# Kernel tuning notes

Hardware: AMD Instinct MI355X
Metric: run time of the kernel (lower is better)

## Reference

```python
import jax, jax.numpy as jnp
import numpy as np

N = 8192          # points
M = 3             # point dimension
K_ORDER = 4       # tensor order k
C = 64            # input_in_channel
KNN = 16          # n_neighbors
NEG_SLOPE = 0.2
EPS = 1e-6


def vn_leaky_relu(v, U, neg_slope=NEG_SLOPE, eps=EPS):
    """Vector-neuron LeakyReLU. v: (n, T, C), U: (C, C) learned direction map."""
    d = jnp.einsum('ntc,cd->ntd', v, U)
    dot = jnp.sum(v * d, axis=1, keepdims=True)        # (n,1,C)
    dn2 = jnp.sum(d * d, axis=1, keepdims=True)        # (n,1,C)
    proj = (dot / (dn2 + eps)) * d
    return neg_slope * v + (1.0 - neg_slope) * jnp.where(dot >= 0, v, v - proj)


def contract_pairs(x, w, k):
    """Learned combination of all pairwise traces.
    x: (n, m,...,m (k axes), C); w: (k*(k-1)//2, C). Returns order k-2 tensor."""
    pairs = [(a, b) for a in range(1, k + 1) for b in range(a + 1, k + 1)]
    acc = None
    for i, (a, b) in enumerate(pairs):
        t = jnp.trace(x, axis1=a, axis2=b)             # (n, m^(k-2)..., C)
        acc = t * w[i] if acc is None else acc + t * w[i]
    return acc


def setup_inputs() -> dict:
    key = jax.random.key(0)
    ks = jax.random.split(key, 8)
    s1 = 1.0 / np.sqrt(C)
    s2 = 1.0 / np.sqrt(2 * C)
    return {
        'x': jax.random.normal(ks[0], (N, M), dtype=jnp.float32),
        'kron_W': jax.random.normal(ks[1], (K_ORDER, C, C), dtype=jnp.float32) * s1,
        'kron_U': jax.random.normal(ks[2], (K_ORDER, C, C), dtype=jnp.float32) * s1,
        'contr_w4': jax.random.normal(ks[3], (6, 2 * C), dtype=jnp.float32) * s2,
        'contr_W': jax.random.normal(ks[4], (2 * C, 2 * C), dtype=jnp.float32) * s2,
        'contr_U': jax.random.normal(ks[5], (2 * C, 2 * C), dtype=jnp.float32) * s2,
        'contr_w2': jax.random.normal(ks[6], (1, 2 * C), dtype=jnp.float32) * s2,
    }


def reference(x, kron_W, kron_U, contr_w4, contr_W, contr_U, contr_w2):
    n, m = x.shape
    c = kron_W.shape[-1]
    # --- brute-force kNN on x (replaces sklearn fit/kneighbors; self included,
    # static because dynamic_knn=False) ---
    sq = jnp.sum(x * x, axis=1)
    d2 = sq[:, None] + sq[None, :] - 2.0 * (x @ x.T)   # (n,n)
    _, idx = jax.lax.top_k(-d2, KNN)                   # (n,KNN) neighbor indices
    xg = x[idx]                                        # (n,KNN,m) gathered coords
    # --- Kronecker stage: v_{t+1}[i] = mean_{j in N(i)} x_j (x) v_t[j] ---
    v = jnp.ones((n, 1, c), dtype=x.dtype)
    for t in range(kron_W.shape[0]):
        vg = v[idx]                                    # (n,KNN,m^t,c)
        v = jnp.einsum('nka,nkbc->nabc', xg, vg) / KNN # (n,m,m^t,c)
        v = v.reshape(n, -1, c)                        # (n,m^(t+1),c)
        v = v @ kron_W[t]                              # CustomLinear (no bias)
        v = vn_leaky_relu(v, kron_U[t])
    # --- mean pooling + concat (pool_type=mean) ---
    g = jnp.mean(v, axis=0, keepdims=True)
    v = jnp.concatenate([v, jnp.broadcast_to(g, v.shape)], axis=2)  # (n,m^k,2c)
    c2 = 2 * c
    k = kron_W.shape[0]
    h = v.reshape((n,) + (m,) * k + (c2,))             # (n,3,3,3,3,2c)
    # --- contraction stage: k=4 -> 2 -> 0 ---
    h = contract_pairs(h, contr_w4, k)                 # (n,m,m,2c)
    h = h.reshape(n, m * m, c2) @ contr_W              # CustomLinear
    h = vn_leaky_relu(h, contr_U)
    h = h.reshape(n, m, m, c2)
    out = contract_pairs(h, contr_w2, 2)               # (n,2c)
    return out
```

## Files before the change

kernel.cpp:

```cpp
#include <hip/hip_runtime.h>
#include <math.h>

#define NPTS 8192
#define KNB  16
#define C1   64
#define C2   128
#define NEG  0.2f
#define VEPS 1e-6f
#define NCH  32
#define CHSZ (NPTS/NCH)

__device__ __forceinline__ unsigned long long expand10(unsigned v) {
    unsigned long long r = v & 0x3FFu;
    r = (r | (r << 16)) & 0x030000FFULL;
    r = (r | (r <<  8)) & 0x0300F00FULL;
    r = (r | (r <<  4)) & 0x030C30C3ULL;
    r = (r | (r <<  2)) & 0x09249249ULL;
    return r;
}

__global__ __launch_bounds__(256) void keys_kernel(const float* __restrict__ x,
                                                   unsigned long long* __restrict__ keys)
{
    const int i = blockIdx.x * 256 + threadIdx.x;
    auto cell = [](float v) -> unsigned {
        float t = (v + 6.f) * (1024.f / 12.f);
        int c = (int)t;
        c = c < 0 ? 0 : (c > 1023 ? 1023 : c);
        return (unsigned)c;
    };
    const unsigned long long m = expand10(cell(x[3*i+0]))
                               | (expand10(cell(x[3*i+1])) << 1)
                               | (expand10(cell(x[3*i+2])) << 2);
    keys[i] = (m << 13) | (unsigned long long)i;
}

__global__ __launch_bounds__(256) void rank_zero(int* __restrict__ rk)
{
    rk[blockIdx.x * 256 + threadIdx.x] = 0;
}

__global__ __launch_bounds__(256) void rank_part(const unsigned long long* __restrict__ keys,
                                                 int* __restrict__ rk)
{
    __shared__ unsigned long long sk[1024];
    const int slice = blockIdx.x & 7;
    const int qg    = blockIdx.x >> 3;
    for (int j = threadIdx.x; j < 1024; j += 256) sk[j] = keys[slice*1024 + j];
    __syncthreads();
    const int i = qg*256 + threadIdx.x;
    const unsigned long long mine = keys[i];
    int r = 0;
    for (int j = 0; j < 1024; j += 4)
        r += (int)(sk[j] < mine) + (int)(sk[j+1] < mine)
           + (int)(sk[j+2] < mine) + (int)(sk[j+3] < mine);
    atomicAdd(&rk[i], r);
}

__global__ __launch_bounds__(256) void rank_scatter(const int* __restrict__ rk,
                                                    const float* __restrict__ x,
                                                    float* __restrict__ xp,
                                                    int* __restrict__ perm)
{
    const int i = blockIdx.x * 256 + threadIdx.x;
    const int r = rk[i];
    perm[r] = i;
    xp[3*r+0] = x[3*i+0]; xp[3*r+1] = x[3*i+1]; xp[3*r+2] = x[3*i+2];
}

__global__ __launch_bounds__(256) void knn_part(const float* __restrict__ x,
                                                unsigned long long* __restrict__ parts)
{
    __shared__ __align__(16) float4 cpt[CHSZ];
    __shared__ unsigned long long sbuf[256 * 9];

    const int tid   = threadIdx.x;
    const int chunk = blockIdx.x & (NCH - 1);
    const int qg    = blockIdx.x >> 5;
    const int j0    = chunk * CHSZ;

    cpt[tid] = make_float4(x[3*(j0+tid)+0], x[3*(j0+tid)+1], x[3*(j0+tid)+2], 0.f);
    const int q = qg * 256 + tid;
    const float qx = x[3*q+0], qy = x[3*q+1], qz = x[3*q+2];

    float thrF;
    {
        int lo = q - 7; lo = lo < 0 ? 0 : (lo > NPTS-16 ? NPTS-16 : lo);
        float mx = 0.f;
#pragma unroll
        for (int s = 0; s < 16; ++s) {
            const float dx = qx - x[3*(lo+s)+0];
            const float dy = qy - x[3*(lo+s)+1];
            const float dz = qz - x[3*(lo+s)+2];
            mx = fmaxf(mx, fmaf(dx, dx, fmaf(dy, dy, dz*dz)));
        }
        thrF = mx * 1.0002f;
    }
    __syncthreads();

    unsigned long long bd[16];
#pragma unroll
    for (int r = 0; r < 16; ++r) bd[r] = ~0ull;
    int cnt = 0;
    unsigned long long* mybuf = sbuf + tid * 9;

    auto flush = [&]() {
#pragma unroll
        for (int s = 0; s < 8; ++s) {
            if (s < cnt) {
                const unsigned long long k = mybuf[s];
                if (k < bd[15]) {
#pragma unroll
                    for (int p2 = 15; p2 > 0; --p2) {
                        const bool sh = k < bd[p2-1];
                        const bool pl = k < bd[p2];
                        bd[p2] = sh ? bd[p2-1] : (pl ? k : bd[p2]);
                    }
                    if (k < bd[0]) bd[0] = k;
                }
            }
        }
        cnt = 0;
        if (bd[15] != ~0ull) {
            const double dub = __longlong_as_double((long long)(bd[15] | 8191ull));
            thrF = fminf(thrF, (float)dub * 1.0001f);
        }
    };

    for (int jj = 0; jj < CHSZ; jj += 4) {
        const float4 p0 = cpt[jj+0];
        const float4 p1 = cpt[jj+1];
        const float4 p2 = cpt[jj+2];
        const float4 p3 = cpt[jj+3];
#pragma unroll
        for (int u = 0; u < 4; ++u) {
            const float4 p = (u==0) ? p0 : (u==1) ? p1 : (u==2) ? p2 : p3;
            const float dx = qx - p.x, dy = qy - p.y, dz = qz - p.z;
            const float d2f = fmaf(dx, dx, fmaf(dy, dy, dz*dz));
            if (d2f <= thrF) {
                const double ddx = (double)dx, ddy = (double)dy, ddz = (double)dz;
                const double d2 = ddx*ddx + ddy*ddy + ddz*ddz;
                const unsigned long long key =
                    (((unsigned long long)__double_as_longlong(d2)) & ~8191ull)
                    | (unsigned long long)(j0 + jj + u);
                if (key < bd[15]) { mybuf[cnt] = key; ++cnt; }
            }
        }
        if (__any(cnt >= 5)) flush();
    }
    flush();

#pragma unroll
    for (int r = 0; r < 16; ++r)
        parts[((size_t)chunk * KNB + r) * NPTS + q] = bd[r];
}

__global__ __launch_bounds__(256) void knn_merge(const unsigned long long* __restrict__ parts,
                                                 int* __restrict__ idx_out)
{
    __shared__ unsigned char heads[256][NCH];
    const int tid = threadIdx.x;
    const int q = blockIdx.x * 256 + tid;
    unsigned char* h = heads[tid];
#pragma unroll
    for (int c = 0; c < NCH; ++c) h[c] = 0;
    for (int r = 0; r < KNB; ++r) {
        unsigned long long best = ~0ull; int bc = 0;
#pragma unroll
        for (int c = 0; c < NCH; ++c) {
            const unsigned long long k = parts[((size_t)c * KNB + h[c]) * NPTS + q];
            if (k < best) { best = k; bc = c; }
        }
        h[bc]++;
        idx_out[q*KNB + r] = (int)(best & 8191ull);
    }
}

__global__ __launch_bounds__(256) void prep_kernel(const float* __restrict__ kW,
                                                   const float* __restrict__ kU,
                                                   float* __restrict__ scol,
                                                   float* __restrict__ bcat)
{
    __shared__ float sW[64*64];
    __shared__ float sS[64];
    const int t = blockIdx.x;
    const int tid = threadIdx.x;
    if (t == 0) {
        for (int e = tid; e < 64*64; e += 256) sW[e] = kW[e];
        __syncthreads();
        if (tid < 64) {
            float s = 0.f;
            for (int j = 0; j < 64; ++j) s += sW[j*64 + tid];
            sS[tid] = s;
        }
        __syncthreads();
        if (tid < 64) {
            float s2 = 0.f;
            for (int j = 0; j < 64; ++j) s2 = fmaf(sS[j], kU[j*64 + tid], s2);
            scol[tid]      = sS[tid];
            scol[64 + tid] = s2;
        }
    } else {
        const float* W = kW + t*4096;
        const float* U = kU + t*4096;
        for (int e = tid; e < 64*64; e += 256) sW[e] = W[e];
        __syncthreads();
        float* B = bcat + (size_t)(t-1)*64*128;
        for (int o = tid; o < 64*64; o += 256) {
            const int j = o >> 6, c = o & 63;
            float s = 0.f;
            for (int l = 0; l < 64; ++l) s = fmaf(sW[j*64 + l], U[l*64 + c], s);
            B[j*128 + c]      = sW[j*64 + c];
            B[j*128 + 64 + c] = s;
        }
    }
}

__global__ __launch_bounds__(256) void step1_kernel(const float* __restrict__ xp,
                                                    const int* __restrict__ idxs,
                                                    const float* __restrict__ scol,
                                                    float* __restrict__ R1)
{
    const int pt = blockIdx.x * 256 + threadIdx.x;
    float mx0 = 0.f, mx1 = 0.f, mx2 = 0.f;
#pragma unroll
    for (int k = 0; k < KNB; ++k) {
        const int id = idxs[pt*KNB + k];
        mx0 += xp[3*id+0]; mx1 += xp[3*id+1]; mx2 += xp[3*id+2];
    }
    const float inv = 1.0f / KNB;
    mx0 *= inv; mx1 *= inv; mx2 *= inv;
    const float S2 = mx0*mx0 + mx1*mx1 + mx2*mx2;
    float* op = R1 + (size_t)pt * 192;
    for (int c = 0; c < 64; ++c) {
        const float sc = scol[c], su = scol[64 + c];
        const float dt = S2 * sc * su;
        const float dn = S2 * su * su;
        const float m  = (dt < 0.f) ? 0.8f * dt / (dn + VEPS) : 0.f;
        const float rc = fmaf(-m, su, sc);
        op[c]       = mx0 * rc;
        op[64 + c]  = mx1 * rc;
        op[128 + c] = mx2 * rc;
    }
}

#define FMA4(ar, b0, b1, b2, b3, acc) \
    acc.x = fmaf(ar.x,b0.x, fmaf(ar.y,b1.x, fmaf(ar.z,b2.x, fmaf(ar.w,b3.x, acc.x)))); \
    acc.y = fmaf(ar.x,b0.y, fmaf(ar.y,b1.y, fmaf(ar.z,b2.y, fmaf(ar.w,b3.y, acc.y)))); \
    acc.z = fmaf(ar.x,b0.z, fmaf(ar.y,b1.z, fmaf(ar.z,b2.z, fmaf(ar.w,b3.z, acc.z)))); \
    acc.w = fmaf(ar.x,b0.w, fmaf(ar.y,b1.w, fmaf(ar.z,b2.w, fmaf(ar.w,b3.w, acc.w))));

__global__ __launch_bounds__(256) void zgemm_kernel(const float* __restrict__ R,
                                                    const float* __restrict__ Bcat,
                                                    float* __restrict__ YwZ)
{
    constexpr int SA = 68;
    __shared__ __align__(16) float sA[64*SA];
    __shared__ __align__(16) float sB[64*128];
    const int tid = threadIdx.x;
    const size_t row0 = (size_t)blockIdx.x * 64;

    for (int e4 = tid; e4 < 1024; e4 += 256) {
        const int r = e4 >> 4, c4 = (e4 & 15) * 4;
        *reinterpret_cast<float4*>(sA + r*SA + c4) =
            *reinterpret_cast<const float4*>(R + (row0 + r)*64 + c4);
    }
    for (int e4 = tid; e4 < 2048; e4 += 256) {
        const int j = e4 >> 5, c4 = (e4 & 31) * 4;
        *reinterpret_cast<float4*>(sB + j*128 + c4) =
            *reinterpret_cast<const float4*>(Bcat + j*128 + c4);
    }
    __syncthreads();

    const int rg = tid >> 5;
    const int d  = (tid & 31) * 4;
    float4 acc0={0,0,0,0},acc1=acc0,acc2=acc0,acc3=acc0,acc4=acc0,acc5=acc0,acc6=acc0,acc7=acc0;
    for (int c = 0; c < 64; c += 4) {
        const float4 b0 = *reinterpret_cast<const float4*>(sB + (c+0)*128 + d);
        const float4 b1 = *reinterpret_cast<const float4*>(sB + (c+1)*128 + d);
        const float4 b2 = *reinterpret_cast<const float4*>(sB + (c+2)*128 + d);
        const float4 b3 = *reinterpret_cast<const float4*>(sB + (c+3)*128 + d);
        float4 a;
        a = *reinterpret_cast<const float4*>(sA + (rg*8+0)*SA + c); FMA4(a,b0,b1,b2,b3,acc0);
        a = *reinterpret_cast<const float4*>(sA + (rg*8+1)*SA + c); FMA4(a,b0,b1,b2,b3,acc1);
        a = *reinterpret_cast<const float4*>(sA + (rg*8+2)*SA + c); FMA4(a,b0,b1,b2,b3,acc2);
        a = *reinterpret_cast<const float4*>(sA + (rg*8+3)*SA + c); FMA4(a,b0,b1,b2,b3,acc3);
        a = *reinterpret_cast<const float4*>(sA + (rg*8+4)*SA + c); FMA4(a,b0,b1,b2,b3,acc4);
        a = *reinterpret_cast<const float4*>(sA + (rg*8+5)*SA + c); FMA4(a,b0,b1,b2,b3,acc5);
        a = *reinterpret_cast<const float4*>(sA + (rg*8+6)*SA + c); FMA4(a,b0,b1,b2,b3,acc6);
        a = *reinterpret_cast<const float4*>(sA + (rg*8+7)*SA + c); FMA4(a,b0,b1,b2,b3,acc7);
    }
    float* op = YwZ + (row0 + rg*8)*128 + d;
    *reinterpret_cast<float4*>(op + 0*128) = acc0;
    *reinterpret_cast<float4*>(op + 1*128) = acc1;
    *reinterpret_cast<float4*>(op + 2*128) = acc2;
    *reinterpret_cast<float4*>(op + 3*128) = acc3;
    *reinterpret_cast<float4*>(op + 4*128) = acc4;
    *reinterpret_cast<float4*>(op + 5*128) = acc5;
    *reinterpret_cast<float4*>(op + 6*128) = acc6;
    *reinterpret_cast<float4*>(op + 7*128) = acc7;
}

template<int PINP, int TT>
__global__ __launch_bounds__(256) void gather_kernel(
    const float* __restrict__ xp, const int* __restrict__ idxs,
    const float* __restrict__ yz,
    float* __restrict__ Rout,
    int ppb)
{
    constexpr int PCW = PINP * 128;
    constexpr int NSL = PCW / 4;
    constexpr int TC  = TT * 64;

    __shared__ __align__(16) float buf[TT * 128];
    __shared__ int   sIds[KNB];
    __shared__ float sXg[KNB*3];
    __shared__ float pdt[4][64], pdn[4][64], msc[64];

    const int tid   = threadIdx.x;
    const int slots = gridDim.x >> 3;
    const int xcd   = blockIdx.x & 7;
    const int slot  = blockIdx.x >> 3;
    const int base  = xcd * slots * ppb;

    for (int pi = 0; pi < ppb; ++pi) {
        const int pt = base + pi * slots + slot;
        if (tid < KNB) {
            const int id = idxs[pt*KNB + tid];
            sIds[tid] = id;
            sXg[tid*3+0] = xp[3*id+0];
            sXg[tid*3+1] = xp[3*id+1];
            sXg[tid*3+2] = xp[3*id+2];
        }
        __syncthreads();

        float xr[KNB*3];
#pragma unroll
        for (int e = 0; e < KNB*3; ++e) xr[e] = sXg[e];

        for (int sl = tid; sl < NSL; sl += 256) {
            const int b  = sl >> 5;
            const int cc = (sl & 31) * 4;
            float4 s0 = {0,0,0,0}, s1 = s0, s2 = s0;
#pragma unroll
            for (int k = 0; k < KNB; ++k) {
                const float4 val = *reinterpret_cast<const float4*>(
                    yz + (size_t)sIds[k]*PCW + b*128 + cc);
                const float xa = xr[k*3+0], xb = xr[k*3+1], xc = xr[k*3+2];
                s0.x=fmaf(xa,val.x,s0.x); s0.y=fmaf(xa,val.y,s0.y);
                s0.z=fmaf(xa,val.z,s0.z); s0.w=fmaf(xa,val.w,s0.w);
                s1.x=fmaf(xb,val.x,s1.x); s1.y=fmaf(xb,val.y,s1.y);
                s1.z=fmaf(xb,val.z,s1.z); s1.w=fmaf(xb,val.w,s1.w);
                s2.x=fmaf(xc,val.x,s2.x); s2.y=fmaf(xc,val.y,s2.y);
                s2.z=fmaf(xc,val.z,s2.z); s2.w=fmaf(xc,val.w,s2.w);
            }
            const float inv = 1.0f / KNB;
            s0.x*=inv; s0.y*=inv; s0.z*=inv; s0.w*=inv;
            s1.x*=inv; s1.y*=inv; s1.z*=inv; s1.w*=inv;
            s2.x*=inv; s2.y*=inv; s2.z*=inv; s2.w*=inv;
            *reinterpret_cast<float4*>(buf + (0*PINP + b)*128 + cc) = s0;
            *reinterpret_cast<float4*>(buf + (1*PINP + b)*128 + cc) = s1;
            *reinterpret_cast<float4*>(buf + (2*PINP + b)*128 + cc) = s2;
        }
        __syncthreads();
        {
            const int c = tid & 63, g = tid >> 6;
            float dt = 0.f, dn = 0.f;
            for (int t = g; t < TT; t += 4) {
                const float vv = buf[t*128 + c], dd = buf[t*128 + 64 + c];
                dt = fmaf(vv, dd, dt); dn = fmaf(dd, dd, dn);
            }
            pdt[g][c] = dt; pdn[g][c] = dn;
        }
        __syncthreads();
        if (tid < 64) {
            const float dt = pdt[0][tid]+pdt[1][tid]+pdt[2][tid]+pdt[3][tid];
            const float dn = pdn[0][tid]+pdn[1][tid]+pdn[2][tid]+pdn[3][tid];
            msc[tid] = (dt < 0.f) ? 0.8f * dt / (dn + VEPS) : 0.f;
        }
        __syncthreads();
        {
            float* op = Rout + (size_t)pt * TC;
            for (int e = tid; e < TC; e += 256) {
                const int t = e >> 6, c = e & 63;
                op[e] = fmaf(-msc[c], buf[t*128 + 64 + c], buf[t*128 + c]);
            }
        }
        __syncthreads();
    }
}

__global__ __launch_bounds__(256) void gather4_kernel(
    const float* __restrict__ xp, const int* __restrict__ idxs,
    const float* __restrict__ yz,
    const float* __restrict__ w4,
    float* __restrict__ hv, float* __restrict__ gpart,
    int ppb)
{
    constexpr int TT = 81;
    constexpr int CH = 32;
    constexpr int NG = (TT*CH + 255) / 256;

    __shared__ __align__(16) float buf[TT * 64];
    __shared__ int   sIds[KNB];
    __shared__ float sXg[KNB*3];
    __shared__ float pdt[8][CH], pdn[8][CH], msc[CH];

    const int tid   = threadIdx.x;
    const int xcd   = blockIdx.x & 7;
    const int r2    = blockIdx.x >> 3;
    const int half  = r2 & 1;
    const int slot  = r2 >> 1;
    const int slots = gridDim.x >> 4;
    const int base0 = xcd * slots * ppb;
    const int c0    = half * CH;
    const int eff   = xcd * slots + slot;

    float gacc[NG];
#pragma unroll
    for (int i = 0; i < NG; ++i) gacc[i] = 0.f;

    for (int pi = 0; pi < ppb; ++pi) {
        const int pt = base0 + pi * slots + slot;
        if (tid < KNB) {
            const int id = idxs[pt*KNB + tid];
            sIds[tid] = id;
            sXg[tid*3+0] = xp[3*id+0];
            sXg[tid*3+1] = xp[3*id+1];
            sXg[tid*3+2] = xp[3*id+2];
        }
        __syncthreads();

        float xr[KNB*3];
#pragma unroll
        for (int e = 0; e < KNB*3; ++e) xr[e] = sXg[e];

        for (int sl = tid; sl < 27*16; sl += 256) {
            const int b  = sl >> 4;
            const int qq = sl & 15;
            const int src = b*128 + ((qq < 8) ? (c0 + qq*4) : (64 + c0 + (qq-8)*4));
            const int dst = (qq < 8) ? qq*4 : (32 + (qq-8)*4);
            float4 s0 = {0,0,0,0}, s1 = s0, s2 = s0;
#pragma unroll
            for (int k = 0; k < KNB; ++k) {
                const float4 val = *reinterpret_cast<const float4*>(
                    yz + (size_t)sIds[k]*3456 + src);
                const float xa = xr[k*3+0], xb = xr[k*3+1], xc = xr[k*3+2];
                s0.x=fmaf(xa,val.x,s0.x); s0.y=fmaf(xa,val.y,s0.y);
                s0.z=fmaf(xa,val.z,s0.z); s0.w=fmaf(xa,val.w,s0.w);
                s1.x=fmaf(xb,val.x,s1.x); s1.y=fmaf(xb,val.y,s1.y);
                s1.z=fmaf(xb,val.z,s1.z); s1.w=fmaf(xb,val.w,s1.w);
                s2.x=fmaf(xc,val.x,s2.x); s2.y=fmaf(xc,val.y,s2.y);
                s2.z=fmaf(xc,val.z,s2.z); s2.w=fmaf(xc,val.w,s2.w);
            }
            const float inv = 1.0f / KNB;
            s0.x*=inv; s0.y*=inv; s0.z*=inv; s0.w*=inv;
            s1.x*=inv; s1.y*=inv; s1.z*=inv; s1.w*=inv;
            s2.x*=inv; s2.y*=inv; s2.z*=inv; s2.w*=inv;
            *reinterpret_cast<float4*>(buf + (0*27 + b)*64 + dst) = s0;
            *reinterpret_cast<float4*>(buf + (1*27 + b)*64 + dst) = s1;
            *reinterpret_cast<float4*>(buf + (2*27 + b)*64 + dst) = s2;
        }
        __syncthreads();
        {
            const int cc = tid & 31, g = tid >> 5;
            float dt = 0.f, dn = 0.f;
            for (int t = g; t < TT; t += 8) {
                const float vv = buf[t*64 + cc], dd = buf[t*64 + 32 + cc];
                dt = fmaf(vv, dd, dt); dn = fmaf(dd, dd, dn);
            }
            pdt[g][cc] = dt; pdn[g][cc] = dn;
        }
        __syncthreads();
        if (tid < CH) {
            float dt = 0.f, dn = 0.f;
#pragma unroll
            for (int g = 0; g < 8; ++g) { dt += pdt[g][tid]; dn += pdn[g][tid]; }
            msc[tid] = (dt < 0.f) ? 0.8f * dt / (dn + VEPS) : 0.f;
        }
        __syncthreads();
#pragma unroll
        for (int i = 0; i < NG; ++i) {
            const int e = i*256 + tid;
            if (e < TT*CH) {
                const int t = e >> 5, cc = e & 31;
                const float v = fmaf(-msc[cc], buf[t*64 + 32 + cc], buf[t*64 + cc]);
                buf[t*64 + cc] = v;
                gacc[i] += v;
            }
        }
        __syncthreads();
        for (int e = tid; e < 9*CH; e += 256) {
            const int pq = e >> 5, cc = e & 31;
            const int p = pq / 3, qq = pq - 3*p;
            const int c = c0 + cc;
            float tr0=0,tr1=0,tr2=0,tr3=0,tr4=0,tr5=0;
#pragma unroll
            for (int r = 0; r < 3; ++r) {
                tr0 += buf[(r*36 + p*3 + qq )*64 + cc];
                tr1 += buf[(r*30 + p*9 + qq )*64 + cc];
                tr2 += buf[(r*28 + p*9 + qq*3)*64 + cc];
                tr3 += buf[(p*27 + r*12 + qq )*64 + cc];
                tr4 += buf[(p*27 + r*10 + qq*3)*64 + cc];
                tr5 += buf[(p*27 + qq*9 + r*4 )*64 + cc];
            }
            hv[(size_t)pt*576 + pq*64 + c] =
                  w4[0*C2 + c]*tr0 + w4[1*C2 + c]*tr1 + w4[2*C2 + c]*tr2
                + w4[3*C2 + c]*tr3 + w4[4*C2 + c]*tr4 + w4[5*C2 + c]*tr5;
        }
        __syncthreads();
    }
    float* gp = gpart + (size_t)eff * 5184;
#pragma unroll
    for (int i = 0; i < NG; ++i) {
        const int e = i*256 + tid;
        if (e < TT*CH) {
            const int t = e >> 5, cc = e & 31;
            gp[t*64 + c0 + cc] = gacc[i];
        }
    }
}

__global__ __launch_bounds__(256) void reduce_g_kernel(const float* __restrict__ gpart,
                                                       float* __restrict__ g)
{
    __shared__ float red[256];
    const int el = threadIdx.x & 15, pg = threadIdx.x >> 4;
    const int e = blockIdx.x * 16 + el;
    float s = 0.f;
    for (int p = pg; p < 1024; p += 16) s += gpart[(size_t)p * (81*C1) + e];
    red[threadIdx.x] = s;
    __syncthreads();
    for (int st = 8; st > 0; st >>= 1) {
        if (pg < st) red[el + 16*pg] += red[el + 16*(pg+st)];
        __syncthreads();
    }
    if (pg == 0) g[e] = red[el] * (1.0f/NPTS);
}

__global__ __launch_bounds__(256) void hgw_kernel(const float* __restrict__ g,
                                                  const float* __restrict__ w4,
                                                  const float* __restrict__ cW,
                                                  float* __restrict__ hgW)
{
    __shared__ float gs[81*C1];
    __shared__ float hg[9*C1];
    const int tid = threadIdx.x;
    for (int e = tid; e < 81*C1; e += 256) gs[e] = g[e];
    __syncthreads();
    for (int e = tid; e < 9*C1; e += 256) {
        const int pq = e >> 6, c = e & 63;
        const int p = pq / 3, qq = pq - 3*p;
        float tr0=0,tr1=0,tr2=0,tr3=0,tr4=0,tr5=0;
#pragma unroll
        for (int r = 0; r < 3; ++r) {
            tr0 += gs[(r*36 + p*3 + qq ) * C1 + c];
            tr1 += gs[(r*30 + p*9 + qq ) * C1 + c];
            tr2 += gs[(r*28 + p*9 + qq*3) * C1 + c];
            tr3 += gs[(p*27 + r*12 + qq ) * C1 + c];
            tr4 += gs[(p*27 + r*10 + qq*3) * C1 + c];
            tr5 += gs[(p*27 + qq*9 + r*4 ) * C1 + c];
        }
        hg[e] = w4[0*C2 + 64 + c]*tr0 + w4[1*C2 + 64 + c]*tr1 + w4[2*C2 + 64 + c]*tr2
              + w4[3*C2 + 64 + c]*tr3 + w4[4*C2 + 64 + c]*tr4 + w4[5*C2 + 64 + c]*tr5;
    }
    __syncthreads();
    for (int o = tid; o < 9*C2; o += 256) {
        const int t = o >> 7, c = o & 127;
        float s = 0.f;
        for (int j = 0; j < C1; ++j) s = fmaf(hg[t*C1 + j], cW[(C1+j)*C2 + c], s);
        hgW[o] = s;
    }
}

__global__ __launch_bounds__(256) void contract_kernel(const float* __restrict__ hv,
                                                       const float* __restrict__ hgW,
                                                       const float* __restrict__ cW,
                                                       const float* __restrict__ cU,
                                                       const float* __restrict__ w2,
                                                       const int* __restrict__ perm,
                                                       float* __restrict__ out,
                                                       int ppb)
{
    constexpr int S0 = C1 + 4;
    constexpr int SH = C2 + 4;
    __shared__ __align__(16) float h0[36*S0];
    __shared__ __align__(16) float h1[36*SH];
    __shared__ __align__(16) float h2[36*SH];
    __shared__ __align__(16) float hgs[9*C2];
    __shared__ int sPerm[4];

    const int tid = threadIdx.x;
    for (int e = tid; e < 9*C2; e += 256) hgs[e] = hgW[e];
    __syncthreads();

    const int iters = ppb >> 2;
    for (int it = 0; it < iters; ++it) {
        const int base = blockIdx.x * ppb + it * 4;
        if (tid < 4) sPerm[tid] = perm[base + tid];
        for (int e = tid; e < 4*9*C1; e += 256) {
            const int pt = e / 576, rem = e - pt*576;
            const int t = rem >> 6, c = rem & 63;
            h0[(pt*9 + t)*S0 + c] = hv[(size_t)(base+pt)*576 + rem];
        }
        __syncthreads();
        for (int u = tid; u < 9*32; u += 256) {
            const int tg = u >> 5;
            const int d  = (u & 31) * 4;
            const int r0 = tg*4;
            float4 acc0 = *reinterpret_cast<const float4*>(hgs + ((r0+0)%9)*C2 + d);
            float4 acc1 = *reinterpret_cast<const float4*>(hgs + ((r0+1)%9)*C2 + d);
            float4 acc2 = *reinterpret_cast<const float4*>(hgs + ((r0+2)%9)*C2 + d);
            float4 acc3 = *reinterpret_cast<const float4*>(hgs + ((r0+3)%9)*C2 + d);
            for (int c = 0; c < C1; c += 4) {
                const float4 a0 = *reinterpret_cast<const float4*>(h0 + (r0+0)*S0 + c);
                const float4 a1 = *reinterpret_cast<const float4*>(h0 + (r0+1)*S0 + c);
                const float4 a2 = *reinterpret_cast<const float4*>(h0 + (r0+2)*S0 + c);
                const float4 a3 = *reinterpret_cast<const float4*>(h0 + (r0+3)*S0 + c);
                const float4 b0 = *reinterpret_cast<const float4*>(cW + (c+0)*C2 + d);
                const float4 b1 = *reinterpret_cast<const float4*>(cW + (c+1)*C2 + d);
                const float4 b2 = *reinterpret_cast<const float4*>(cW + (c+2)*C2 + d);
                const float4 b3 = *reinterpret_cast<const float4*>(cW + (c+3)*C2 + d);
                FMA4(a0, b0, b1, b2, b3, acc0);
                FMA4(a1, b0, b1, b2, b3, acc1);
                FMA4(a2, b0, b1, b2, b3, acc2);
                FMA4(a3, b0, b1, b2, b3, acc3);
            }
            *reinterpret_cast<float4*>(h1 + (r0+0)*SH + d) = acc0;
            *reinterpret_cast<float4*>(h1 + (r0+1)*SH + d) = acc1;
            *reinterpret_cast<float4*>(h1 + (r0+2)*SH + d) = acc2;
            *reinterpret_cast<float4*>(h1 + (r0+3)*SH + d) = acc3;
        }
        __syncthreads();
        for (int u = tid; u < 9*32; u += 256) {
            const int tg = u >> 5;
            const int d  = (u & 31) * 4;
            const int r0 = tg*4;
            float4 acc0 = {0,0,0,0}, acc1 = acc0, acc2 = acc0, acc3 = acc0;
            for (int c = 0; c < C2; c += 4) {
                const float4 a0 = *reinterpret_cast<const float4*>(h1 + (r0+0)*SH + c);
                const float4 a1 = *reinterpret_cast<const float4*>(h1 + (r0+1)*SH + c);
                const float4 a2 = *reinterpret_cast<const float4*>(h1 + (r0+2)*SH + c);
                const float4 a3 = *reinterpret_cast<const float4*>(h1 + (r0+3)*SH + c);
                const float4 b0 = *reinterpret_cast<const float4*>(cU + (c+0)*C2 + d);
                const float4 b1 = *reinterpret_cast<const float4*>(cU + (c+1)*C2 + d);
                const float4 b2 = *reinterpret_cast<const float4*>(cU + (c+2)*C2 + d);
                const float4 b3 = *reinterpret_cast<const float4*>(cU + (c+3)*C2 + d);
                FMA4(a0, b0, b1, b2, b3, acc0);
                FMA4(a1, b0, b1, b2, b3, acc1);
                FMA4(a2, b0, b1, b2, b3, acc2);
                FMA4(a3, b0, b1, b2, b3, acc3);
            }
            *reinterpret_cast<float4*>(h2 + (r0+0)*SH + d) = acc0;
            *reinterpret_cast<float4*>(h2 + (r0+1)*SH + d) = acc1;
            *reinterpret_cast<float4*>(h2 + (r0+2)*SH + d) = acc2;
            *reinterpret_cast<float4*>(h2 + (r0+3)*SH + d) = acc3;
        }
        __syncthreads();
#pragma unroll
        for (int p2 = 0; p2 < 2; ++p2) {
            const int pair = tid + 256*p2;
            const int pt = pair >> 7, c = pair & 127;
            float dt = 0.f, dn = 0.f;
            for (int t = 0; t < 9; ++t) {
                const float vv = h1[(pt*9+t)*SH + c], dd = h2[(pt*9+t)*SH + c];
                dt = fmaf(vv, dd, dt); dn = fmaf(dd, dd, dn);
            }
            const float m = (dt < 0.f) ? 0.8f * dt / (dn + VEPS) : 0.f;
            float s = 0.f;
#pragma unroll
            for (int r = 0; r < 3; ++r) {
                const int t = r * 4;
                s += fmaf(-m, h2[(pt*9+t)*SH + c], h1[(pt*9+t)*SH + c]);
            }
            out[(size_t)sPerm[pt]*C2 + c] = w2[c] * s;
        }
        __syncthreads();
    }
}

extern "C" void kernel_launch(void* const* d_in, const int* in_sizes, int n_in,
                              void* d_out, int out_size, void* d_ws, size_t ws_size,
                              hipStream_t stream)
{
    (void)in_sizes; (void)n_in; (void)out_size; (void)ws_size;
    const float* x  = (const float*)d_in[0];
    const float* kW = (const float*)d_in[1];
    const float* kU = (const float*)d_in[2];
    const float* w4 = (const float*)d_in[3];
    const float* cW = (const float*)d_in[4];
    const float* cU = (const float*)d_in[5];
    const float* w2 = (const float*)d_in[6];
    float* out = (float*)d_out;

    char* ws = (char*)d_ws;
    size_t off = 0;
    auto alloc = [&](size_t bytes) -> void* {
        void* p = ws + off; off += (bytes + 255) & ~(size_t)255; return p;
    };
    int*   idx   = (int*)  alloc((size_t)NPTS*KNB*4);
    float* xp    = (float*)alloc((size_t)NPTS*3*4);
    unsigned long long* keys = (unsigned long long*)alloc((size_t)NPTS*8);
    int*   perm  = (int*)  alloc((size_t)NPTS*4);
    int*   rk    = (int*)  alloc((size_t)NPTS*4);
    float* scol  = (float*)alloc(128*4);
    float* bcat  = (float*)alloc((size_t)3*64*128*4);
    float* R1    = (float*)alloc((size_t)NPTS*3*C1*4);
    float* YwZ2  = (float*)alloc((size_t)NPTS*3*C2*4);
    float* R2    = (float*)alloc((size_t)NPTS*9*C1*4);
    float* YwZ3  = (float*)alloc((size_t)NPTS*9*C2*4);
    float* R3    = (float*)alloc((size_t)NPTS*27*C1*4);
    float* YwZ4  = (float*)alloc((size_t)NPTS*27*C2*4);
    float* g     = (float*)alloc((size_t)81*C1*4);
    float* hgW   = (float*)alloc((size_t)9*C2*4);

    float* hv    = R1;
    float* gpart = R2;
    unsigned long long* parts = (unsigned long long*)YwZ4;

    keys_kernel <<<NPTS/256, 256, 0, stream>>>(x, keys);
    rank_zero   <<<NPTS/256, 256, 0, stream>>>(rk);
    rank_part   <<<256, 256, 0, stream>>>(keys, rk);
    rank_scatter<<<NPTS/256, 256, 0, stream>>>(rk, x, xp, perm);
    knn_part    <<<32*NCH, 256, 0, stream>>>(xp, parts);
    knn_merge   <<<NPTS/256, 256, 0, stream>>>(parts, idx);
    prep_kernel <<<4, 256, 0, stream>>>(kW, kU, scol, bcat);
    step1_kernel<<<NPTS/256, 256, 0, stream>>>(xp, idx, scol, R1);

    zgemm_kernel<<<NPTS*3/64,  256, 0, stream>>>(R1, bcat,            YwZ2);
    gather_kernel<3, 9>  <<<1024, 256, 0, stream>>>(xp, idx, YwZ2, R2, 8);
    zgemm_kernel<<<NPTS*9/64,  256, 0, stream>>>(R2, bcat + 8192,     YwZ3);
    gather_kernel<9, 27> <<<1024, 256, 0, stream>>>(xp, idx, YwZ3, R3, 8);
    zgemm_kernel<<<NPTS*27/64, 256, 0, stream>>>(R3, bcat + 16384,    YwZ4);
    gather4_kernel<<<2048, 256, 0, stream>>>(xp, idx, YwZ4, w4, hv, gpart, 8);

    reduce_g_kernel<<<324, 256, 0, stream>>>(gpart, g);
    hgw_kernel<<<1, 256, 0, stream>>>(g, w4, cW, hgW);
    contract_kernel<<<1024, 256, 0, stream>>>(hv, hgW, cW, cU, w2, perm, out, 8);
}
```

Measured before the change: 715.5 us.

## Restructure gather4 thread mapping, pad LDS rows, and double gather grid sizes

The gather4 kernel now has each thread compute both the value and direction vectors for one basis slot and channel quad, so the VN dot and norm partial sums come straight from registers. This removes a separate LDS pass and one barrier. LDS rows are padded from 64 to 68 floats to reduce bank conflicts. Grid sizes for gather kernels are doubled with half the points per block to raise parallelism, and reduce_g reads twice as many partials. In exchange, 40 of 256 threads sit idle during accumulation, and the partial-sum buffer and its reduction are larger.

```diff
diff --git a/kernel.cpp b/kernel.cpp
--- a/kernel.cpp
+++ b/kernel.cpp
@@ -390,6 +390,10 @@
     }
 }
 
+#define FMAQS(acc, s, val) \
+    acc.x = fmaf(s, val.x, acc.x); acc.y = fmaf(s, val.y, acc.y); \
+    acc.z = fmaf(s, val.z, acc.z); acc.w = fmaf(s, val.w, acc.w);
+
 __global__ __launch_bounds__(256) void gather4_kernel(
     const float* __restrict__ xp, const int* __restrict__ idxs,
     const float* __restrict__ yz,
@@ -399,12 +403,14 @@
 {
     constexpr int TT = 81;
     constexpr int CH = 32;
+    constexpr int SB = 68;
     constexpr int NG = (TT*CH + 255) / 256;
 
-    __shared__ __align__(16) float buf[TT * 64];
+    __shared__ __align__(16) float buf[TT * SB];
     __shared__ int   sIds[KNB];
     __shared__ float sXg[KNB*3];
-    __shared__ float pdt[8][CH], pdn[8][CH], msc[CH];
+    __shared__ float pdt[27][33], pdn[27][33];
+    __shared__ float msc[CH];
 
     const int tid   = threadIdx.x;
     const int xcd   = blockIdx.x & 7;
@@ -416,6 +422,12 @@
     const int c0    = half * CH;
     const int eff   = xcd * slots + slot;
 
+    const int ub  = tid >> 3;
+    const int ucq = tid & 7;
+    const bool act = (ub < 27);
+    const int srcV = ub*128 + c0 + ucq*4;
+    const int srcD = srcV + 64;
+
     float gacc[NG];
 #pragma unroll
     for (int i = 0; i < NG; ++i) gacc[i] = 0.f;
@@ -431,51 +443,47 @@
         }
         __syncthreads();
 
-        float xr[KNB*3];
-#pragma unroll
-        for (int e = 0; e < KNB*3; ++e) xr[e] = sXg[e];
-
-        for (int sl = tid; sl < 27*16; sl += 256) {
-            const int b  = sl >> 4;
-            const int qq = sl & 15;
-            const int src = b*128 + ((qq < 8) ? (c0 + qq*4) : (64 + c0 + (qq-8)*4));
-            const int dst = (qq < 8) ? qq*4 : (32 + (qq-8)*4);
-            float4 s0 = {0,0,0,0}, s1 = s0, s2 = s0;
+        if (act) {
+            float4 vA[3], dA[3];
+#pragma unroll
+            for (int a = 0; a < 3; ++a) { vA[a] = make_float4(0,0,0,0); dA[a] = vA[a]; }
 #pragma unroll
             for (int k = 0; k < KNB; ++k) {
-                const float4 val = *reinterpret_cast<const float4*>(
-                    yz + (size_t)sIds[k]*3456 + src);
-                const float xa = xr[k*3+0], xb = xr[k*3+1], xc = xr[k*3+2];
-                s0.x=fmaf(xa,val.x,s0.x); s0.y=fmaf(xa,val.y,s0.y);
-                s0.z=fmaf(xa,val.z,s0.z); s0.w=fmaf(xa,val.w,s0.w);
-                s1.x=fmaf(xb,val.x,s1.x); s1.y=fmaf(xb,val.y,s1.y);
-                s1.z=fmaf(xb,val.z,s1.z); s1.w=fmaf(xb,val.w,s1.w);
-                s2.x=fmaf(xc,val.x,s2.x); s2.y=fmaf(xc,val.y,s2.y);
-                s2.z=fmaf(xc,val.z,s2.z); s2.w=fmaf(xc,val.w,s2.w);
+                const float* rowp = yz + (size_t)sIds[k]*3456;
+                const float4 vq = *reinterpret_cast<const float4*>(rowp + srcV);
+                const float4 dq = *reinterpret_cast<const float4*>(rowp + srcD);
+                const float xa = sXg[k*3+0], xb = sXg[k*3+1], xc = sXg[k*3+2];
+                FMAQS(vA[0], xa, vq) FMAQS(vA[1], xb, vq) FMAQS(vA[2], xc, vq)
+                FMAQS(dA[0], xa, dq) FMAQS(dA[1], xb, dq) FMAQS(dA[2], xc, dq)
             }
             const float inv = 1.0f / KNB;
-            s0.x*=inv; s0.y*=inv; s0.z*=inv; s0.w*=inv;
-            s1.x*=inv; s1.y*=inv; s1.z*=inv; s1.w*=inv;
-            s2.x*=inv; s2.y*=inv; s2.z*=inv; s2.w*=inv;
-            *reinterpret_cast<float4*>(buf + (0*27 + b)*64 + dst) = s0;
-            *reinterpret_cast<float4*>(buf + (1*27 + b)*64 + dst) = s1;
-            *reinterpret_cast<float4*>(buf + (2*27 + b)*64 + dst) = s2;
-        }
-        __syncthreads();
-        {
-            const int cc = tid & 31, g = tid >> 5;
-            float dt = 0.f, dn = 0.f;
-            for (int t = g; t < TT; t += 8) {
-                const float vv = buf[t*64 + cc], dd = buf[t*64 + 32 + cc];
-                dt = fmaf(vv, dd, dt); dn = fmaf(dd, dd, dn);
-            }
-            pdt[g][cc] = dt; pdn[g][cc] = dn;
+            float4 dt4 = make_float4(0,0,0,0), dn4 = dt4;
+#pragma unroll
+            for (int a = 0; a < 3; ++a) {
+                vA[a].x*=inv; vA[a].y*=inv; vA[a].z*=inv; vA[a].w*=inv;
+                dA[a].x*=inv; dA[a].y*=inv; dA[a].z*=inv; dA[a].w*=inv;
+                dt4.x = fmaf(vA[a].x, dA[a].x, dt4.x);
+                dt4.y = fmaf(vA[a].y, dA[a].y, dt4.y);
+                dt4.z = fmaf(vA[a].z, dA[a].z, dt4.z);
+                dt4.w = fmaf(vA[a].w, dA[a].w, dt4.w);
+                dn4.x = fmaf(dA[a].x, dA[a].x, dn4.x);
+                dn4.y = fmaf(dA[a].y, dA[a].y, dn4.y);
+                dn4.z = fmaf(dA[a].z, dA[a].z, dn4.z);
+                dn4.w = fmaf(dA[a].w, dA[a].w, dn4.w);
+                float* bp = buf + (a*27 + ub)*SB;
+                *reinterpret_cast<float4*>(bp + ucq*4)      = vA[a];
+                *reinterpret_cast<float4*>(bp + 32 + ucq*4) = dA[a];
+            }
+            pdt[ub][ucq*4+0] = dt4.x; pdt[ub][ucq*4+1] = dt4.y;
+            pdt[ub][ucq*4+2] = dt4.z; pdt[ub][ucq*4+3] = dt4.w;
+            pdn[ub][ucq*4+0] = dn4.x; pdn[ub][ucq*4+1] = dn4.y;
+            pdn[ub][ucq*4+2] = dn4.z; pdn[ub][ucq*4+3] = dn4.w;
         }
         __syncthreads();
         if (tid < CH) {
             float dt = 0.f, dn = 0.f;
 #pragma unroll
-            for (int g = 0; g < 8; ++g) { dt += pdt[g][tid]; dn += pdn[g][tid]; }
+            for (int b2 = 0; b2 < 27; ++b2) { dt += pdt[b2][tid]; dn += pdn[b2][tid]; }
             msc[tid] = (dt < 0.f) ? 0.8f * dt / (dn + VEPS) : 0.f;
         }
         __syncthreads();
@@ -484,8 +492,8 @@
             const int e = i*256 + tid;
             if (e < TT*CH) {
                 const int t = e >> 5, cc = e & 31;
-                const float v = fmaf(-msc[cc], buf[t*64 + 32 + cc], buf[t*64 + cc]);
-                buf[t*64 + cc] = v;
+                const float v = fmaf(-msc[cc], buf[t*SB + 32 + cc], buf[t*SB + cc]);
+                buf[t*SB + cc] = v;
                 gacc[i] += v;
             }
         }
@@ -497,12 +505,12 @@
             float tr0=0,tr1=0,tr2=0,tr3=0,tr4=0,tr5=0;
 #pragma unroll
             for (int r = 0; r < 3; ++r) {
-                tr0 += buf[(r*36 + p*3 + qq )*64 + cc];
-                tr1 += buf[(r*30 + p*9 + qq )*64 + cc];
-                tr2 += buf[(r*28 + p*9 + qq*3)*64 + cc];
-                tr3 += buf[(p*27 + r*12 + qq )*64 + cc];
-                tr4 += buf[(p*27 + r*10 + qq*3)*64 + cc];
-                tr5 += buf[(p*27 + qq*9 + r*4 )*64 + cc];
+                tr0 += buf[(r*36 + p*3 + qq )*SB + cc];
+                tr1 += buf[(r*30 + p*9 + qq )*SB + cc];
+                tr2 += buf[(r*28 + p*9 + qq*3)*SB + cc];
+                tr3 += buf[(p*27 + r*12 + qq )*SB + cc];
+                tr4 += buf[(p*27 + r*10 + qq*3)*SB + cc];
+                tr5 += buf[(p*27 + qq*9 + r*4 )*SB + cc];
             }
             hv[(size_t)pt*576 + pq*64 + c] =
                   w4[0*C2 + c]*tr0 + w4[1*C2 + c]*tr1 + w4[2*C2 + c]*tr2
@@ -528,7 +536,7 @@
     const int el = threadIdx.x & 15, pg = threadIdx.x >> 4;
     const int e = blockIdx.x * 16 + el;
     float s = 0.f;
-    for (int p = pg; p < 1024; p += 16) s += gpart[(size_t)p * (81*C1) + e];
+    for (int p = pg; p < 2048; p += 16) s += gpart[(size_t)p * (81*C1) + e];
     red[threadIdx.x] = s;
     __syncthreads();
     for (int st = 8; st > 0; st >>= 1) {
@@ -728,11 +736,11 @@
     step1_kernel<<<NPTS/256, 256, 0, stream>>>(xp, idx, scol, R1);
 
     zgemm_kernel<<<NPTS*3/64,  256, 0, stream>>>(R1, bcat,            YwZ2);
-    gather_kernel<3, 9>  <<<1024, 256, 0, stream>>>(xp, idx, YwZ2, R2, 8);
+    gather_kernel<3, 9>  <<<2048, 256, 0, stream>>>(xp, idx, YwZ2, R2, 4);
     zgemm_kernel<<<NPTS*9/64,  256, 0, stream>>>(R2, bcat + 8192,     YwZ3);
-    gather_kernel<9, 27> <<<1024, 256, 0, stream>>>(xp, idx, YwZ3, R3, 8);
+    gather_kernel<9, 27> <<<2048, 256, 0, stream>>>(xp, idx, YwZ3, R3, 4);
     zgemm_kernel<<<NPTS*27/64, 256, 0, stream>>>(R3, bcat + 16384,    YwZ4);
-    gather4_kernel<<<2048, 256, 0, stream>>>(xp, idx, YwZ4, w4, hv, gpart, 8);
+    gather4_kernel<<<4096, 256, 0, stream>>>(xp, idx, YwZ4, w4, hv, gpart, 4);
 
     reduce_g_kernel<<<324, 256, 0, stream>>>(gpart, g);
     hgw_kernel<<<1, 256, 0, stream>>>(g, w4, cW, hgW);
```

New measurement: 690.5 us. -3.5%, faster.
